# Kernel optimization log

Hardware: AMD Instinct MI355X
Metric: run time of the kernel (lower is better)

Reference implementation:

```python
import jax, jax.numpy as jnp
import numpy as np

T, B, D = 512, 16, 2048


def setup_inputs() -> dict:
    key = jax.random.key(0)
    k1, k2, k3, k4, k5 = jax.random.split(key, 5)
    scale = 1.0 / np.sqrt(D)  # keep tanh pre-activations in a sane range
    return {
        "h0": jax.random.normal(k1, (B, D), dtype=jnp.float32),
        "x": jax.random.normal(k2, (T, B, D), dtype=jnp.float32),
        "Wx": jax.random.normal(k3, (D, D), dtype=jnp.float32) * scale,
        "Wh": jax.random.normal(k4, (D, D), dtype=jnp.float32) * scale,
        "Wo": jax.random.normal(k5, (D, D), dtype=jnp.float32) * scale,
    }


def reference(h0, x, Wx, Wh, Wo):
    # ONNX Scan with 1 state var, 1 scan input (axis 0, forward direction),
    # 1 scan output (stacked on axis 0, forward direction), 3 outer vars.
    # Body: h' = tanh(x_t @ Wx + h @ Wh); y_t = h' @ Wo
    def step(h, x_t):
        h_new = jnp.tanh(x_t @ Wx + h @ Wh)   # [B, D]
        y_t = h_new @ Wo                      # [B, D]
        return h_new, y_t

    h_final, ys = jax.lax.scan(step, h0, x)   # ys: [T, B, D]
    return (h_final, ys)
```

## Files before the change

### kernel.cpp

```cpp
#include <hip/hip_runtime.h>
#include <hip/hip_bf16.h>

#define DD 2048
#define TT 512
#define NBLK 64
#define HF_SLOT 32768
#define KT 64
#define FSTRIDE 16

typedef __attribute__((ext_vector_type(4))) float  f32x4;
typedef __attribute__((ext_vector_type(8))) short  bf16x8;
typedef __attribute__((ext_vector_type(8))) unsigned short u16x8;
typedef unsigned short ushort_t;
typedef unsigned long long u64_t;

__device__ __forceinline__ void gld_lds16(const void* g, void* l) {
    __builtin_amdgcn_global_load_lds(
        (const __attribute__((address_space(1))) unsigned int*)g,
        (__attribute__((address_space(3))) unsigned int*)l, 16, 0, 0);
}

__device__ __forceinline__ ushort_t f2bf(float v) {
    __hip_bfloat16 h = __float2bfloat16(v);
    return *(ushort_t*)&h;
}

__device__ __forceinline__ u64_t llc_load64(const u64_t* p) {
    return __hip_atomic_load(p, __ATOMIC_RELAXED, __HIP_MEMORY_SCOPE_AGENT);
}
__device__ __forceinline__ void llc_store64(u64_t* p, u64_t v) {
    __hip_atomic_store(p, v, __ATOMIC_RELAXED, __HIP_MEMORY_SCOPE_AGENT);
}
__device__ __forceinline__ unsigned llc_load32(const unsigned* p) {
    return __hip_atomic_load(p, __ATOMIC_RELAXED, __HIP_MEMORY_SCOPE_AGENT);
}
__device__ __forceinline__ float llc_loadf(const float* p) {
    return __hip_atomic_load(p, __ATOMIC_RELAXED, __HIP_MEMORY_SCOPE_AGENT);
}

__global__ void conv_frag(const float* __restrict__ src, ushort_t* __restrict__ dst) {
    int id = blockIdx.x * 256 + threadIdx.x;
    int l  = id & 63;
    int sk = (id >> 6) & 63;
    int mt = id >> 12;
    const float* s = src + (size_t)(mt * 16 + (l & 15)) * DD + sk * 32 + ((l >> 4) * 8);
    float4 a = *(const float4*)s;
    float4 b = *(const float4*)(s + 4);
    u16x8 r;
    r[0] = f2bf(a.x); r[1] = f2bf(a.y); r[2] = f2bf(a.z); r[3] = f2bf(a.w);
    r[4] = f2bf(b.x); r[5] = f2bf(b.y); r[6] = f2bf(b.z); r[7] = f2bf(b.w);
    *(u16x8*)(dst + (size_t)id * 8) = r;
}

__global__ void conv_wt(const float* __restrict__ W, ushort_t* __restrict__ Wt) {
    int id = blockIdx.x * 256 + threadIdx.x;
    int n  = id & (DD - 1);
    int k8 = id >> 11;
    u16x8 r;
#pragma unroll
    for (int j = 0; j < 8; ++j)
        r[j] = f2bf(W[(size_t)(k8 * 8 + j) * DD + n]);
    *(u16x8*)(Wt + (size_t)n * DD + k8 * 8) = r;
}

__global__ __launch_bounds__(256) void gemm_frag(
    const ushort_t* __restrict__ Af, const ushort_t* __restrict__ Bt,
    float* __restrict__ C) {
    __shared__ ushort_t lA[8 * 64 * 8];
    __shared__ ushort_t lB[8 * 64 * 8];
    int tid = threadIdx.x;
    int w = tid >> 6, l = tid & 63;
    int wm = w >> 1, wn = w & 1;
    int quad = l >> 4, col = l & 15;
    int mt0 = blockIdx.x * 8;
    int n0  = blockIdx.y * 128;

    f32x4 acc[4][4] = {};

    for (int sk = 0; sk < KT; ++sk) {
        __syncthreads();
#pragma unroll
        for (int q = 0; q < 2; ++q) {
            int i = w * 2 + q;
            const ushort_t* ga = Af + ((size_t)((mt0 + i) * 64 + sk) * 64 + l) * 8;
            gld_lds16(ga, &lA[i * 512]);
            int jt = i;
            const ushort_t* gb = Bt + (size_t)(n0 + jt * 16 + col) * DD + sk * 32 + quad * 8;
            gld_lds16(gb, &lB[jt * 512]);
        }
        __syncthreads();
        bf16x8 af[4], bf[4];
#pragma unroll
        for (int i = 0; i < 4; ++i) af[i] = *(const bf16x8*)&lA[((wm * 4 + i) * 64 + l) * 8];
#pragma unroll
        for (int j = 0; j < 4; ++j) bf[j] = *(const bf16x8*)&lB[((wn * 4 + j) * 64 + l) * 8];
#pragma unroll
        for (int i = 0; i < 4; ++i)
#pragma unroll
            for (int j = 0; j < 4; ++j)
                acc[i][j] = __builtin_amdgcn_mfma_f32_16x16x32_bf16(af[i], bf[j], acc[i][j], 0, 0, 0);
    }

#pragma unroll
    for (int i = 0; i < 4; ++i)
#pragma unroll
        for (int j = 0; j < 4; ++j) {
            int rg0 = (mt0 + wm * 4 + i) * 16 + quad * 4;
            int cg  = n0 + (wn * 4 + j) * 16 + col;
#pragma unroll
            for (int r = 0; r < 4; ++r)
                C[(size_t)(rg0 + r) * DD + cg] = acc[i][j][r];
        }
}

__global__ __launch_bounds__(256, 1) void rnn_fused(
    const ushort_t* __restrict__ Wht,
    const ushort_t* __restrict__ Wot,
    ushort_t* __restrict__ Hf,
    const float* __restrict__ A32,
    float* __restrict__ out,
    unsigned* __restrict__ flags) {
    __shared__ ushort_t lW[4 * 16 * 2 * 512];
    __shared__ float scr[2048];
    __shared__ ushort_t hstage[512];
    int tid = threadIdx.x;
    int w = tid >> 6, l = tid & 63;
    int quad = l >> 4, col = l & 15;
    bool is_rnn = blockIdx.x < NBLK;
    int b = is_rnn ? blockIdx.x : blockIdx.x - NBLK;
    int c0 = b * 32;
    float* ys = out + HF_SLOT;

    const ushort_t* Wsrc = is_rnn ? Wht : Wot;
#pragma unroll
    for (int s = 0; s < 16; ++s) {
        int sk = w * 16 + s;
#pragma unroll
        for (int jt = 0; jt < 2; ++jt) {
            const ushort_t* gb = Wsrc + (size_t)(c0 + jt * 16 + col) * DD + sk * 32 + quad * 8;
            gld_lds16(gb, &lW[((w * 16 + s) * 2 + jt) << 9]);
        }
    }
    __syncthreads();

    for (int t = 1; t <= TT; ++t) {
        float av[4];
        if (is_rnn && w < 2) {
#pragma unroll
            for (int r = 0; r < 4; ++r)
                av[r] = llc_loadf(&A32[(size_t)((t - 1) * 16 + quad * 4 + r) * DD + c0 + w * 16 + col]);
        }

        unsigned tgt = is_rnn ? (unsigned)(t - 1) : (unsigned)t;
        if (w == 3) {
            unsigned f;
            do {
                f = llc_load32(&flags[l * FSTRIDE]);
            } while (!__all((int)(f >= tgt)));
        }
        __syncthreads();

        const ushort_t* hsrc = Hf + (size_t)(is_rnn ? t - 1 : t) * HF_SLOT;
        bf16x8 hv[16];
#pragma unroll
        for (int s = 0; s < 16; ++s) {
            int sk = w * 16 + s;
            const u64_t* p = (const u64_t*)(hsrc + (size_t)(sk * 64 + l) * 8);
            union { u64_t q[2]; bf16x8 v; } u;
            u.q[0] = llc_load64(p);
            u.q[1] = llc_load64(p + 1);
            hv[s] = u.v;
        }

        f32x4 acc0 = {0.f, 0.f, 0.f, 0.f};
        f32x4 acc1 = {0.f, 0.f, 0.f, 0.f};
#pragma unroll
        for (int s = 0; s < 16; ++s) {
            bf16x8 w0 = *(const bf16x8*)&lW[(((w * 16 + s) * 2 + 0) << 9) + l * 8];
            bf16x8 w1 = *(const bf16x8*)&lW[(((w * 16 + s) * 2 + 1) << 9) + l * 8];
            acc0 = __builtin_amdgcn_mfma_f32_16x16x32_bf16(hv[s], w0, acc0, 0, 0, 0);
            acc1 = __builtin_amdgcn_mfma_f32_16x16x32_bf16(hv[s], w1, acc1, 0, 0, 0);
        }
        *(f32x4*)&scr[((w * 2 + 0) * 64 + l) * 4] = acc0;
        *(f32x4*)&scr[((w * 2 + 1) * 64 + l) * 4] = acc1;
        __syncthreads();

        if (w < 2) {
            int jt = w;
            f32x4 p0 = *(f32x4*)&scr[((0 * 2 + jt) * 64 + l) * 4];
            f32x4 p1 = *(f32x4*)&scr[((1 * 2 + jt) * 64 + l) * 4];
            f32x4 p2 = *(f32x4*)&scr[((2 * 2 + jt) * 64 + l) * 4];
            f32x4 p3 = *(f32x4*)&scr[((3 * 2 + jt) * 64 + l) * 4];
            int lc = jt * 16 + col;
            if (is_rnn) {
                int q2 = lc >> 3, jj = lc & 7;
#pragma unroll
                for (int r = 0; r < 4; ++r) {
                    int m = quad * 4 + r;
                    float x = p0[r] + p1[r] + p2[r] + p3[r] + av[r];
                    float e2 = __expf(-2.f * fabsf(x));
                    float th = copysignf((1.f - e2) / (1.f + e2), x);
                    hstage[(q2 * 16 + m) * 8 + jj] = f2bf(th);
                    if (t == TT) out[(size_t)m * DD + c0 + lc] = th;
                }
            } else {
#pragma unroll
                for (int r = 0; r < 4; ++r) {
                    int m = quad * 4 + r;
                    float y = p0[r] + p1[r] + p2[r] + p3[r];
                    ys[(size_t)((t - 1) * 16 + m) * DD + c0 + lc] = y;
                }
            }
        }

        if (is_rnn) {
            __syncthreads();
            if (w == 0) {
                u64_t* dst = (u64_t*)(Hf + (size_t)t * HF_SLOT + (size_t)(c0 >> 5) * 512);
                const u64_t* s = (const u64_t*)hstage;
                llc_store64(dst + l,      s[l]);
                llc_store64(dst + 64 + l, s[64 + l]);
                __builtin_amdgcn_s_waitcnt(0);
                if (l == 0)
                    __hip_atomic_store(&flags[b * FSTRIDE], (unsigned)t,
                                       __ATOMIC_RELAXED, __HIP_MEMORY_SCOPE_AGENT);
            }
        }
    }
}

extern "C" void kernel_launch(void* const* d_in, const int* in_sizes, int n_in,
                              void* d_out, int out_size, void* d_ws, size_t ws_size,
                              hipStream_t stream) {
    const float* h0 = (const float*)d_in[0];
    const float* x  = (const float*)d_in[1];
    const float* Wx = (const float*)d_in[2];
    const float* Wh = (const float*)d_in[3];
    const float* Wo = (const float*)d_in[4];
    float* out = (float*)d_out;

    char* ws = (char*)d_ws;
    unsigned* flags = (unsigned*)ws;
    ushort_t* Hf  = (ushort_t*)(ws + 4096);
    ushort_t* Xf  = Hf + HF_SLOT;
    size_t hf_bytes = (size_t)(TT + 1) * HF_SLOT * 2;
    ushort_t* Wxt = (ushort_t*)(ws + 4096 + hf_bytes);
    ushort_t* Wht = Wxt + (size_t)DD * DD;
    ushort_t* Wot = Wht + (size_t)DD * DD;
    float* A32 = out + HF_SLOT;

    hipMemsetAsync(d_ws, 0, 4096, stream);

    conv_frag<<<8192, 256, 0, stream>>>(x, Xf);
    conv_frag<<<16, 256, 0, stream>>>(h0, Hf);
    conv_wt<<<2048, 256, 0, stream>>>(Wx, Wxt);
    conv_wt<<<2048, 256, 0, stream>>>(Wh, Wht);
    conv_wt<<<2048, 256, 0, stream>>>(Wo, Wot);

    gemm_frag<<<dim3(64, 16), 256, 0, stream>>>(Xf, Wxt, A32);

    rnn_fused<<<2 * NBLK, 256, 0, stream>>>(Wht, Wot, Hf, A32, out, flags);
}
```

Baseline: 1.914 ms.

## Poll hidden-state data for NaN sentinels instead of waiting on store completion

Fills the per-step hidden-state buffers with a NaN sentinel pattern before the recurrent kernel, and has consumers re-load their h fragments until no sentinel remains. The producer no longer waits for its stores to complete before raising the flag, which removes a full memory-wait from each step's critical path. The flag wait is still present, so the gain depends on how much the dropped waitcnt cost. This adds an extra fill kernel over the whole buffer and relies on the sentinel never appearing as a real bf16 value.

```diff
diff --git a/kernel.cpp b/kernel.cpp
--- a/kernel.cpp
+++ b/kernel.cpp
@@ -7,6 +7,7 @@
 #define HF_SLOT 32768
 #define KT 64
 #define FSTRIDE 16
+#define SENT64 0x7FC07FC07FC07FC0ull
 
 typedef __attribute__((ext_vector_type(4))) float  f32x4;
 typedef __attribute__((ext_vector_type(8))) short  bf16x8;
@@ -61,6 +62,13 @@
     for (int j = 0; j < 8; ++j)
         r[j] = f2bf(W[(size_t)(k8 * 8 + j) * DD + n]);
     *(u16x8*)(Wt + (size_t)n * DD + k8 * 8) = r;
+}
+
+__global__ void fill_sent(u64_t* __restrict__ dst) {
+    size_t id = (size_t)blockIdx.x * 256 + threadIdx.x;
+    u64_t v = SENT64;
+    dst[id * 2]     = v;
+    dst[id * 2 + 1] = v;
 }
 
 __global__ __launch_bounds__(256) void gemm_frag(
@@ -161,14 +169,34 @@
         __syncthreads();
 
         const ushort_t* hsrc = Hf + (size_t)(is_rnn ? t - 1 : t) * HF_SLOT;
-        bf16x8 hv[16];
+        u64_t q0[16], q1[16];
 #pragma unroll
         for (int s = 0; s < 16; ++s) {
             int sk = w * 16 + s;
             const u64_t* p = (const u64_t*)(hsrc + (size_t)(sk * 64 + l) * 8);
+            q0[s] = llc_load64(p);
+            q1[s] = llc_load64(p + 1);
+        }
+        while (true) {
+            bool ok = true;
+#pragma unroll
+            for (int s = 0; s < 16; ++s)
+                ok = ok & (q0[s] != SENT64) & (q1[s] != SENT64);
+            if (__all((int)ok)) break;
+#pragma unroll
+            for (int s = 0; s < 16; ++s) {
+                int sk = w * 16 + s;
+                const u64_t* p = (const u64_t*)(hsrc + (size_t)(sk * 64 + l) * 8);
+                q0[s] = llc_load64(p);
+                q1[s] = llc_load64(p + 1);
+            }
+        }
+        bf16x8 hv[16];
+#pragma unroll
+        for (int s = 0; s < 16; ++s) {
             union { u64_t q[2]; bf16x8 v; } u;
-            u.q[0] = llc_load64(p);
-            u.q[1] = llc_load64(p + 1);
+            u.q[0] = q0[s];
+            u.q[1] = q1[s];
             hv[s] = u.v;
         }
 
@@ -216,11 +244,11 @@
         if (is_rnn) {
             __syncthreads();
             if (w == 0) {
-                u64_t* dst = (u64_t*)(Hf + (size_t)t * HF_SLOT + (size_t)(c0 >> 5) * 512);
+                u64_t* dst = (u64_t*)(Hf + (size_t)t * HF_SLOT + (size_t)b * 512);
                 const u64_t* s = (const u64_t*)hstage;
                 llc_store64(dst + l,      s[l]);
                 llc_store64(dst + 64 + l, s[64 + l]);
-                __builtin_amdgcn_s_waitcnt(0);
+                asm volatile("" ::: "memory");
                 if (l == 0)
                     __hip_atomic_store(&flags[b * FSTRIDE], (unsigned)t,
                                        __ATOMIC_RELAXED, __HIP_MEMORY_SCOPE_AGENT);
@@ -259,5 +287,7 @@
 
     gemm_frag<<<dim3(64, 16), 256, 0, stream>>>(Xf, Wxt, A32);
 
+    fill_sent<<<8192, 256, 0, stream>>>((u64_t*)(Hf + HF_SLOT));
+
     rnn_fused<<<2 * NBLK, 256, 0, stream>>>(Wht, Wot, Hf, A32, out, flags);
 }
```

Measured after the change: 2.086 ms. +9.0%, slower.
